# Optimization experiments

Hardware: AMD Instinct MI355X
Metric: run time of the kernel (lower is better)

Reference implementation:

```python
import jax, jax.numpy as jnp
import numpy as np

NUM_HEADS = 16
DIM = 1024
N_TOKENS = 2048
S0 = 8            # number of frames
P = N_TOKENS // S0  # tokens per frame
B = 1


def setup_inputs() -> dict:
    key = jax.random.key(0)
    ks = jax.random.split(key, 8)
    C = DIM
    x = jax.random.normal(ks[0], (B, N_TOKENS, C), dtype=jnp.float32)
    # nn.Linear-style weights (out_features, in_features), scaled ~1/sqrt(fan_in)
    Wqkv = jax.random.normal(ks[1], (3 * C, C), dtype=jnp.float32) * (C ** -0.5)
    bqkv = jnp.zeros((3 * C,), dtype=jnp.float32)
    Wproj = jax.random.normal(ks[2], (C, C), dtype=jnp.float32) * (C ** -0.5)
    bproj = jnp.zeros((C,), dtype=jnp.float32)
    frame_bias = jax.random.normal(ks[3], (S0, S0), dtype=jnp.float32) * 0.5
    # frame adjacency: random sparsity pattern, diagonal always allowed
    adj = jax.random.bernoulli(ks[4], 0.25, (S0, S0))
    adj = adj | jnp.eye(S0, dtype=bool)
    frame_ids = (jnp.arange(N_TOKENS) // P).astype(jnp.int64)
    is_hub = jax.random.bernoulli(ks[5], 0.05, (N_TOKENS,))
    return {
        'x': x, 'Wqkv': Wqkv, 'bqkv': bqkv, 'Wproj': Wproj, 'bproj': bproj,
        'frame_bias': frame_bias, 'adj': adj, 'frame_ids': frame_ids,
        'is_hub': is_hub,
    }


def _sparse_attention(x, Wqkv, bqkv, Wproj, bproj, frame_bias, adj, frame_ids, is_hub):
    Bx, N, C = x.shape
    H = NUM_HEADS
    D = C // H
    scale = D ** -0.5
    # qkv projection -> q,k,v each [B,H,N,D]
    qkv = x @ Wqkv.T + bqkv                      # [B,N,3C]
    qkv = qkv.reshape(Bx, N, 3, H, D).transpose(2, 0, 3, 1, 4)
    q, k, v = qkv[0], qkv[1], qkv[2]

    # token-level mask derived from frame-level structures (score_mod semantics)
    fi = frame_ids                               # [N]
    adj_allowed = adj[fi[:, None], fi[None, :]]  # [N,N] bool
    same_frame = fi[:, None] == fi[None, :]
    neither_hub = ~(is_hub[:, None] | is_hub[None, :])
    hub_allowed = same_frame | neither_hub       # mask_hub_tokens=True
    allowed = adj_allowed & hub_allowed
    bias = frame_bias[fi[:, None], fi[None, :]]  # soft_mask=True

    scores = jnp.einsum('bhqd,bhkd->bhqk', q, k) * scale
    scores = jnp.where(allowed, scores + bias, -jnp.inf)
    attn = jax.nn.softmax(scores, axis=-1)
    out = jnp.einsum('bhqk,bhkd->bhqd', attn, v)
    out = out.transpose(0, 2, 1, 3).reshape(Bx, N, C)
    return out @ Wproj.T + bproj


def reference(x, Wqkv, bqkv, Wproj, bproj, frame_bias, adj, frame_ids, is_hub):
    return _sparse_attention(x, Wqkv, bqkv, Wproj, bproj, frame_bias,
                             adj, frame_ids, is_hub)
```

## Files before the change

### kernel.cpp

```cpp
#include <hip/hip_runtime.h>
#include <hip/hip_bf16.h>
#include <math.h>

#define NTOK 2048
#define CDIM 1024
#define NHEAD 16
#define HDIM 64

typedef __attribute__((ext_vector_type(8))) short bf16x8;
typedef __attribute__((ext_vector_type(4))) float f32x4;
typedef __attribute__((ext_vector_type(4))) unsigned int u32x4;

__device__ inline unsigned short bf16_rn(float f) {
    unsigned int u = __float_as_uint(f);
    u += 0x7FFFu + ((u >> 16) & 1u);
    return (unsigned short)(u >> 16);
}

template <int N> __device__ inline void waitcnt_vm() {
    if constexpr (N == 0) asm volatile("s_waitcnt vmcnt(0)" ::: "memory");
    else if constexpr (N == 4) asm volatile("s_waitcnt vmcnt(4)" ::: "memory");
    else if constexpr (N == 6) asm volatile("s_waitcnt vmcnt(6)" ::: "memory");
}

__device__ inline void gload16(const void* g, void* l) {
    __builtin_amdgcn_global_load_lds((const __attribute__((address_space(1))) void*)g,
                                     (__attribute__((address_space(3))) void*)l,
                                     16, 0, 0);
}

__global__ __launch_bounds__(256) void conv3(const float* __restrict__ s0, unsigned short* __restrict__ h0, int nb0,
                                             const float* __restrict__ s1, unsigned short* __restrict__ h1, int nb1,
                                             const float* __restrict__ s2, unsigned short* __restrict__ h2) {
    int b = blockIdx.x;
    const float* s;
    unsigned short* hh;
    if (b < nb0) { s = s0; hh = h0; }
    else if (b < nb0 + nb1) { s = s1; hh = h1; b -= nb0; }
    else { s = s2; hh = h2; b -= nb0 + nb1; }
    const int i = b * 256 + threadIdx.x;
    float4 v = ((const float4*)s)[i];
    ushort4 h;
    h.x = bf16_rn(v.x); h.y = bf16_rn(v.y); h.z = bf16_rn(v.z); h.w = bf16_rn(v.w);
    ((ushort4*)hh)[i] = h;
}

template <int BM, int BN, int M, int N, int K, int MODE>
__global__ __launch_bounds__(256) void gemm_mfma(const unsigned short* __restrict__ Ah,
                                                 const unsigned short* __restrict__ Bh,
                                                 const float* __restrict__ bias,
                                                 float* __restrict__ C,
                                                 unsigned short* __restrict__ qfb,
                                                 unsigned short* __restrict__ kfb,
                                                 unsigned short* __restrict__ vfb) {
    constexpr int BK = 64;
    constexpr int FM = BM / 32;
    constexpr int FN = BN / 32;
    constexpr int ASZ = BM * BK;
    constexpr int BSZ = BN * BK;
    constexpr int BUF = ASZ + BSZ;
    __shared__ unsigned short lds[2 * BUF];

    const int tid = threadIdx.x;
    const int lane = tid & 63;
    const int w = tid >> 6;
    const int m0 = blockIdx.y * BM;
    const int n0 = blockIdx.x * BN;
    const int wave_m = (w >> 1) * (BM / 2);
    const int wave_n = (w & 1) * (BN / 2);
    const int lr = lane & 15;
    const int kg_ = lane >> 4;
    const int srow = tid >> 3;
    const int scol = (tid & 7) * 8;

    const size_t aRow = (size_t)(m0 + srow) * K + scol;
    const size_t bRow = (size_t)(n0 + srow) * K + scol;

    f32x4 acc[FM][FN];
#pragma unroll
    for (int i = 0; i < FM; ++i)
#pragma unroll
        for (int j = 0; j < FN; ++j) acc[i][j] = {0.f, 0.f, 0.f, 0.f};

    auto stage = [&](int buf, int k0) {
        unsigned short* bb = lds + buf * BUF;
#pragma unroll
        for (int j = 0; j < BM / 32; ++j)
            gload16(Ah + aRow + (size_t)j * 32 * K + k0, bb + (srow + j * 32) * BK + scol);
#pragma unroll
        for (int j = 0; j < BN / 32; ++j)
            gload16(Bh + bRow + (size_t)j * 32 * K + k0, bb + ASZ + (srow + j * 32) * BK + scol);
    };

    stage(0, 0);
    constexpr int NL = BM / 32 + BN / 32;
    constexpr int NT = K / BK;
    for (int t = 0; t < NT; ++t) {
        const int cur = t & 1;
        if (t + 1 < NT) {
            stage(cur ^ 1, (t + 1) * BK);
            waitcnt_vm<NL>();
        } else {
            waitcnt_vm<0>();
        }
        __builtin_amdgcn_s_barrier();

        const unsigned short* bb = lds + cur * BUF;
        bf16x8 ah[FM][2], bh[FN][2];
#pragma unroll
        for (int f = 0; f < FM; ++f)
#pragma unroll
            for (int ks = 0; ks < 2; ++ks)
                ah[f][ks] = *(const bf16x8*)&bb[(wave_m + f * 16 + lr) * BK + ks * 32 + kg_ * 8];
#pragma unroll
        for (int f = 0; f < FN; ++f)
#pragma unroll
            for (int ks = 0; ks < 2; ++ks)
                bh[f][ks] = *(const bf16x8*)&bb[ASZ + (wave_n + f * 16 + lr) * BK + ks * 32 + kg_ * 8];
        __builtin_amdgcn_s_setprio(1);
#pragma unroll
        for (int ks = 0; ks < 2; ++ks)
#pragma unroll
            for (int fm = 0; fm < FM; ++fm)
#pragma unroll
                for (int fn = 0; fn < FN; ++fn)
                    acc[fm][fn] = __builtin_amdgcn_mfma_f32_16x16x32_bf16(ah[fm][ks], bh[fn][ks], acc[fm][fn], 0, 0, 0);
        __builtin_amdgcn_s_setprio(0);
        asm volatile("" ::: "memory");
        __builtin_amdgcn_s_barrier();
    }

    if constexpr (MODE == 2) {
        float bv[FN];
#pragma unroll
        for (int fn = 0; fn < FN; ++fn) bv[fn] = bias[n0 + wave_n + fn * 16 + lr];
#pragma unroll
        for (int fm = 0; fm < FM; ++fm) {
            const int row0 = m0 + wave_m + fm * 16 + kg_ * 4;
#pragma unroll
            for (int fn = 0; fn < FN; ++fn) {
                const int col = n0 + wave_n + fn * 16 + lr;
#pragma unroll
                for (int r = 0; r < 4; ++r)
                    C[(size_t)(row0 + r) * N + col] = acc[fm][fn][r] + bv[fn];
            }
        }
    } else {
        const int reg = n0 >> 10;
#pragma unroll
        for (int fn = 0; fn < FN; ++fn) {
            const int col = n0 + wave_n + fn * 16 + lr;
            const int head = (col >> 6) & 15;
            const int d = col & 63;
            const float bv = bias[col];
#pragma unroll
            for (int fm = 0; fm < FM; ++fm) {
                const int row0 = m0 + wave_m + fm * 16 + kg_ * 4;
                if (reg == 2) {
                    const int tok = row0;
                    const int tile = tok >> 6;
                    const int t6 = tok & 63;
                    const int c = t6 >> 5;
                    const int t5 = t6 & 31;
                    const int hi = (t5 >> 4) & 1;
                    const int kgv = (t5 >> 2) & 3;
                    const int fd = d >> 4;
                    const int lrv = d & 15;
                    ushort4 pk;
                    pk.x = bf16_rn(acc[fm][fn][0] + bv);
                    pk.y = bf16_rn(acc[fm][fn][1] + bv);
                    pk.z = bf16_rn(acc[fm][fn][2] + bv);
                    pk.w = bf16_rn(acc[fm][fn][3] + bv);
                    const size_t idx = (((size_t)((head * 32 + tile) * 2 + c) * 4 + fd) * 64 +
                                        (kgv * 16 + lrv)) * 8 + hi * 4;
                    *(ushort4*)&vfb[idx] = pk;
                } else if (reg == 1) {
                    const int dc = d >> 5;
                    const int kgq = (d >> 3) & 3;
                    const int e = d & 7;
#pragma unroll
                    for (int r = 0; r < 4; ++r) {
                        const int tok = row0 + r;
                        const int tile = tok >> 6;
                        const int fk = (tok >> 4) & 3;
                        const int lrk = tok & 15;
                        const size_t idx = (((size_t)((head * 32 + tile) * 4 + fk) * 2 + dc) * 64 +
                                            (kgq * 16 + lrk)) * 8 + e;
                        kfb[idx] = bf16_rn(acc[fm][fn][r] + bv);
                    }
                } else {
                    const int dc = d >> 5;
                    const int kgq = (d >> 3) & 3;
                    const int e = d & 7;
#pragma unroll
                    for (int r = 0; r < 4; ++r) {
                        const int tok = row0 + r;
                        const int q16i = tok >> 4;
                        const int lrk = tok & 15;
                        const size_t idx = (((size_t)(head * 128 + q16i) * 2 + dc) * 64 +
                                            (kgq * 16 + lrk)) * 8 + e;
                        qfb[idx] = bf16_rn((acc[fm][fn][r] + bv) * 0.125f);
                    }
                }
            }
        }
    }
}

__global__ __launch_bounds__(128, 4) void attn_mfma(const unsigned short* __restrict__ qfb,
                                                    const unsigned short* __restrict__ kfb,
                                                    const unsigned short* __restrict__ vfb,
                                                    const float* __restrict__ frame_bias,
                                                    const int* __restrict__ adj,
                                                    const int* __restrict__ is_hub,
                                                    unsigned short* __restrict__ ath) {
    __shared__ float sM[64][18];
    __shared__ int sList[32];
    __shared__ float sFB[8];
    __shared__ unsigned long long sHub[32];
    __shared__ int sNT;

    const int bid = blockIdx.x;
    const int r8 = bid & 7, tt = bid >> 3;
    const int q16 = tt & 127, hb = tt >> 7;
    const int h = r8 * 2 + hb;
    const int q0 = q16 * 16;

    const int tid = threadIdx.x;
    const int lane = tid & 63;
    const int w = tid >> 6;
    const int lr = lane & 15;
    const int kg = lane >> 4;
    const int fi = q0 >> 8;

    const unsigned short* qb = qfb + ((size_t)(h * 128 + q16) * 2) * 512;
    bf16x8 qh[2];
    qh[0] = *(const bf16x8*)&qb[lane * 8];
    qh[1] = *(const bf16x8*)&qb[512 + lane * 8];
    const bool hq = is_hub[q0 + lr] != 0;

#pragma unroll
    for (int i = 0; i < 16; ++i) {
        const int t2 = w * 16 + i;
        unsigned long long mb = __ballot(is_hub[t2 * 64 + lane] != 0);
        if (lane == 0) sHub[t2] = mb;
    }
    if (tid < 8) sFB[tid] = frame_bias[fi * 8 + tid];
    if (w == 0) {
        const bool ok = (lane < 32) && (adj[fi * 8 + ((lane & 31) >> 2)] != 0);
        const unsigned long long am = __ballot(ok);
        if (lane == 0) {
            int c = 0;
#pragma unroll 1
            for (int t2 = 0; t2 < 32; ++t2)
                if ((am >> t2) & 1ull) sList[c++] = t2;
            sNT = c;
        }
    }
    __syncthreads();
    const int nt = sNT;

    const unsigned short* kb = kfb + (size_t)(h * 32) * 4096;
    const unsigned short* vb = vfb + (size_t)(h * 32) * 4096;

    float m_i = -INFINITY, l_i = 0.f;
    f32x4 oacc[4];
#pragma unroll
    for (int fd = 0; fd < 4; ++fd) oacc[fd] = {0.f, 0.f, 0.f, 0.f};

#pragma unroll 1
    for (int i = w; i < nt; i += 2) {
        const int tile = sList[i];
        const size_t tbase = (size_t)tile * 4096 + lane * 8;
        const int fj = tile >> 2;
        const bool same = (fj == fi);
        const float biasv = sFB[fj];
        const unsigned long long hubmask = sHub[tile];

        bf16x8 kfr[4][2];
#pragma unroll
        for (int fk = 0; fk < 4; ++fk)
#pragma unroll
            for (int dc = 0; dc < 2; ++dc)
                kfr[fk][dc] = *(const bf16x8*)&kb[tbase + (fk * 2 + dc) * 512];

        f32x4 sacc[4];
#pragma unroll
        for (int fk = 0; fk < 4; ++fk) sacc[fk] = {0.f, 0.f, 0.f, 0.f};
        __builtin_amdgcn_s_setprio(1);
#pragma unroll
        for (int fk = 0; fk < 4; ++fk)
#pragma unroll
            for (int dc = 0; dc < 2; ++dc)
                sacc[fk] = __builtin_amdgcn_mfma_f32_16x16x32_bf16(kfr[fk][dc], qh[dc], sacc[fk], 0, 0, 0);
        __builtin_amdgcn_s_setprio(0);

        bf16x8 vfr[2][4];
#pragma unroll
        for (int c = 0; c < 2; ++c)
#pragma unroll
            for (int fd = 0; fd < 4; ++fd)
                vfr[c][fd] = *(const bf16x8*)&vb[tbase + (c * 4 + fd) * 512];

        float sv[4][4];
        float rmax = -INFINITY;
#pragma unroll
        for (int fk = 0; fk < 4; ++fk)
#pragma unroll
            for (int r = 0; r < 4; ++r) {
                float val = sacc[fk][r] + biasv;
                if (!same) {
                    const int k = fk * 16 + kg * 4 + r;
                    if (hq || ((hubmask >> k) & 1ull)) val = -INFINITY;
                }
                sv[fk][r] = val;
                rmax = fmaxf(rmax, val);
            }
        rmax = fmaxf(rmax, __shfl_xor(rmax, 16));
        rmax = fmaxf(rmax, __shfl_xor(rmax, 32));

        if (!__all(rmax <= m_i + 8.f)) {
            const float mn = fmaxf(m_i, rmax);
            const float alpha = (m_i == -INFINITY) ? 0.f : __expf(m_i - mn);
            m_i = mn;
            l_i *= alpha;
#pragma unroll
            for (int fd = 0; fd < 4; ++fd) {
                oacc[fd][0] *= alpha; oacc[fd][1] *= alpha;
                oacc[fd][2] *= alpha; oacc[fd][3] *= alpha;
            }
        }

        float p4[4][4];
        float psum = 0.f;
#pragma unroll
        for (int fk = 0; fk < 4; ++fk)
#pragma unroll
            for (int r = 0; r < 4; ++r) {
                const float pv = (sv[fk][r] == -INFINITY) ? 0.f : __expf(sv[fk][r] - m_i);
                p4[fk][r] = pv;
                psum += pv;
            }
        psum += __shfl_xor(psum, 16);
        psum += __shfl_xor(psum, 32);
        l_i += psum;

        unsigned int pc[4][2];
#pragma unroll
        for (int fk = 0; fk < 4; ++fk)
#pragma unroll
            for (int rp = 0; rp < 2; ++rp)
                pc[fk][rp] = (unsigned int)bf16_rn(p4[fk][2 * rp]) |
                             ((unsigned int)bf16_rn(p4[fk][2 * rp + 1]) << 16);
        __builtin_amdgcn_s_setprio(1);
#pragma unroll
        for (int c = 0; c < 2; ++c) {
            u32x4 pw = {pc[2 * c][0], pc[2 * c][1], pc[2 * c + 1][0], pc[2 * c + 1][1]};
            bf16x8 pbv = __builtin_bit_cast(bf16x8, pw);
#pragma unroll
            for (int fd = 0; fd < 4; ++fd)
                oacc[fd] = __builtin_amdgcn_mfma_f32_16x16x32_bf16(vfr[c][fd], pbv, oacc[fd], 0, 0, 0);
        }
        __builtin_amdgcn_s_setprio(0);
    }

    if (w == 1) {
        float* mp = &sM[lane][0];
        mp[0] = m_i;
        mp[1] = l_i;
#pragma unroll
        for (int fd = 0; fd < 4; ++fd)
#pragma unroll
            for (int r = 0; r < 4; ++r) mp[2 + fd * 4 + r] = oacc[fd][r];
    }
    __syncthreads();
    if (w == 0) {
        const float mb = sM[lane][0];
        const float lb = sM[lane][1];
        const float m = fmaxf(m_i, mb);
        const float aa = (m_i == -INFINITY) ? 0.f : __expf(m_i - m);
        const float ab = (mb == -INFINITY) ? 0.f : __expf(mb - m);
        const float inv = 1.f / (l_i * aa + lb * ab);
#pragma unroll
        for (int fd = 0; fd < 4; ++fd) {
            ushort4 h4;
            unsigned short hs[4];
#pragma unroll
            for (int r = 0; r < 4; ++r) {
                const float o = (oacc[fd][r] * aa + sM[lane][2 + fd * 4 + r] * ab) * inv;
                hs[r] = bf16_rn(o);
            }
            h4.x = hs[0]; h4.y = hs[1]; h4.z = hs[2]; h4.w = hs[3];
            const size_t idx = (size_t)(q0 + lr) * CDIM + h * 64 + fd * 16 + kg * 4;
            *(ushort4*)&ath[idx] = h4;
        }
    }
}

extern "C" void kernel_launch(void* const* d_in, const int* in_sizes, int n_in,
                              void* d_out, int out_size, void* d_ws, size_t ws_size,
                              hipStream_t stream) {
    const float* x          = (const float*)d_in[0];
    const float* Wqkv       = (const float*)d_in[1];
    const float* bqkv       = (const float*)d_in[2];
    const float* Wproj      = (const float*)d_in[3];
    const float* bproj      = (const float*)d_in[4];
    const float* frame_bias = (const float*)d_in[5];
    const int*   adj        = (const int*)d_in[6];
    const int*   is_hub     = (const int*)d_in[8];
    float* out = (float*)d_out;

    char* ws = (char*)d_ws;
    size_t off = 0;
    auto alloc_us = [&](size_t n) { unsigned short* p = (unsigned short*)(ws + off); off += n * 2; return p; };
    unsigned short* qfb = alloc_us((size_t)NHEAD * NTOK * HDIM);
    unsigned short* kfb = alloc_us((size_t)NHEAD * NTOK * HDIM);
    unsigned short* vfb = alloc_us((size_t)NHEAD * HDIM * NTOK);
    unsigned short* xh  = alloc_us((size_t)NTOK * CDIM);
    unsigned short* wqh = alloc_us((size_t)3 * CDIM * CDIM);
    unsigned short* wph = alloc_us((size_t)CDIM * CDIM);
    unsigned short* ath = alloc_us((size_t)NTOK * CDIM);

    const int nb_x = (NTOK * CDIM / 4) / 256;
    const int nb_wq = (3 * CDIM * CDIM / 4) / 256;
    const int nb_wp = (CDIM * CDIM / 4) / 256;
    conv3<<<nb_x + nb_wq + nb_wp, 256, 0, stream>>>(x, xh, nb_x,
                                                    Wqkv, wqh, nb_wq,
                                                    Wproj, wph);

    gemm_mfma<64, 128, NTOK, 3 * CDIM, CDIM, 1>
        <<<dim3((3 * CDIM) / 128, NTOK / 64), 256, 0, stream>>>(
            xh, wqh, bqkv, nullptr, qfb, kfb, vfb);
    attn_mfma<<<2048, 128, 0, stream>>>(qfb, kfb, vfb,
                                        frame_bias, adj, is_hub, ath);
    gemm_mfma<64, 64, NTOK, CDIM, CDIM, 2>
        <<<dim3(CDIM / 64, NTOK / 64), 256, 0, stream>>>(
            ath, wph, bproj, out, nullptr, nullptr, nullptr);
}
```

Before: 70.12 us.

## Prefetch next K tile in attention loop and stage Q/K epilogue via LDS

The attention loop now double-buffers K fragments, issuing the next tile's K loads before processing the current tile so global load latency overlaps the MFMA and softmax work. Separately, the QKV GEMM epilogue for the Q and K regions first writes the fp32 results to shared memory and then emits packed 8-element bf16 vector stores, replacing scattered 2-byte stores. Both add register or LDS pressure and an extra barrier. The epilogue also assumes the LDS buffer is large enough for the staged tile.

```diff
diff --git a/kernel.cpp b/kernel.cpp
--- a/kernel.cpp
+++ b/kernel.cpp
@@ -147,17 +147,16 @@
         }
     } else {
         const int reg = n0 >> 10;
-#pragma unroll
-        for (int fn = 0; fn < FN; ++fn) {
-            const int col = n0 + wave_n + fn * 16 + lr;
-            const int head = (col >> 6) & 15;
-            const int d = col & 63;
-            const float bv = bias[col];
-#pragma unroll
-            for (int fm = 0; fm < FM; ++fm) {
-                const int row0 = m0 + wave_m + fm * 16 + kg_ * 4;
-                if (reg == 2) {
-                    const int tok = row0;
+        if (reg == 2) {
+#pragma unroll
+            for (int fn = 0; fn < FN; ++fn) {
+                const int col = n0 + wave_n + fn * 16 + lr;
+                const int head = (col >> 6) & 15;
+                const int d = col & 63;
+                const float bv = bias[col];
+#pragma unroll
+                for (int fm = 0; fm < FM; ++fm) {
+                    const int tok = m0 + wave_m + fm * 16 + kg_ * 4;
                     const int tile = tok >> 6;
                     const int t6 = tok & 63;
                     const int c = t6 >> 5;
@@ -174,34 +173,58 @@
                     const size_t idx = (((size_t)((head * 32 + tile) * 2 + c) * 4 + fd) * 64 +
                                         (kgv * 16 + lrv)) * 8 + hi * 4;
                     *(ushort4*)&vfb[idx] = pk;
-                } else if (reg == 1) {
-                    const int dc = d >> 5;
-                    const int kgq = (d >> 3) & 3;
-                    const int e = d & 7;
-#pragma unroll
-                    for (int r = 0; r < 4; ++r) {
-                        const int tok = row0 + r;
-                        const int tile = tok >> 6;
-                        const int fk = (tok >> 4) & 3;
-                        const int lrk = tok & 15;
-                        const size_t idx = (((size_t)((head * 32 + tile) * 4 + fk) * 2 + dc) * 64 +
-                                            (kgq * 16 + lrk)) * 8 + e;
-                        kfb[idx] = bf16_rn(acc[fm][fn][r] + bv);
-                    }
-                } else {
-                    const int dc = d >> 5;
-                    const int kgq = (d >> 3) & 3;
-                    const int e = d & 7;
-#pragma unroll
-                    for (int r = 0; r < 4; ++r) {
-                        const int tok = row0 + r;
-                        const int q16i = tok >> 4;
-                        const int lrk = tok & 15;
-                        const size_t idx = (((size_t)(head * 128 + q16i) * 2 + dc) * 64 +
-                                            (kgq * 16 + lrk)) * 8 + e;
-                        qfb[idx] = bf16_rn((acc[fm][fn][r] + bv) * 0.125f);
-                    }
                 }
+            }
+        } else {
+            float* sOut = (float*)lds;
+            float bv[FN];
+#pragma unroll
+            for (int fn = 0; fn < FN; ++fn) bv[fn] = bias[n0 + wave_n + fn * 16 + lr];
+#pragma unroll
+            for (int fm = 0; fm < FM; ++fm) {
+                const int row0 = wave_m + fm * 16 + kg_ * 4;
+#pragma unroll
+                for (int fn = 0; fn < FN; ++fn) {
+                    const int col = wave_n + fn * 16 + lr;
+#pragma unroll
+                    for (int r = 0; r < 4; ++r)
+                        sOut[(row0 + r) * 132 + col] = acc[fm][fn][r] + bv[fn];
+                }
+            }
+            __syncthreads();
+            const float sc = (reg == 0) ? 0.125f : 1.0f;
+            unsigned short* dp = (reg == 0) ? qfb : kfb;
+            const int tokL = tid >> 2;
+            const int tokG = m0 + tokL;
+            const int lrk = tokG & 15;
+#pragma unroll
+            for (int j = 0; j < 4; ++j) {
+                const int ch = (tid & 3) + j * 4;
+                const int dcol = ch * 8;
+                const int gcol = n0 + dcol;
+                const int head = (gcol >> 6) & 15;
+                const int d = gcol & 63;
+                const int dc = d >> 5;
+                const int kgq = (d >> 3) & 3;
+                float4 v0 = *(float4*)&sOut[tokL * 132 + dcol];
+                float4 v1 = *(float4*)&sOut[tokL * 132 + dcol + 4];
+                bf16x8 pk;
+                pk[0] = (short)bf16_rn(v0.x * sc);
+                pk[1] = (short)bf16_rn(v0.y * sc);
+                pk[2] = (short)bf16_rn(v0.z * sc);
+                pk[3] = (short)bf16_rn(v0.w * sc);
+                pk[4] = (short)bf16_rn(v1.x * sc);
+                pk[5] = (short)bf16_rn(v1.y * sc);
+                pk[6] = (short)bf16_rn(v1.z * sc);
+                pk[7] = (short)bf16_rn(v1.w * sc);
+                size_t idx;
+                if (reg == 1)
+                    idx = (((size_t)((head * 32 + (tokG >> 6)) * 4 + ((tokG >> 4) & 3)) * 2 + dc) * 64 +
+                           (kgq * 16 + lrk)) * 8;
+                else
+                    idx = (((size_t)(head * 128 + (tokG >> 4)) * 2 + dc) * 64 +
+                           (kgq * 16 + lrk)) * 8;
+                *(bf16x8*)&dp[idx] = pk;
             }
         }
     }
@@ -268,22 +291,22 @@
 #pragma unroll
     for (int fd = 0; fd < 4; ++fd) oacc[fd] = {0.f, 0.f, 0.f, 0.f};
 
-#pragma unroll 1
-    for (int i = w; i < nt; i += 2) {
-        const int tile = sList[i];
+    auto loadK = [&](bf16x8 (&kf)[4][2], int tile) {
+        const size_t tb = (size_t)tile * 4096 + lane * 8;
+#pragma unroll
+        for (int fk = 0; fk < 4; ++fk)
+#pragma unroll
+            for (int dc = 0; dc < 2; ++dc)
+                kf[fk][dc] = *(const bf16x8*)&kb[tb + (fk * 2 + dc) * 512];
+    };
+
+    auto procTile = [&](int tile, bf16x8 (&kf)[4][2]) {
         const size_t tbase = (size_t)tile * 4096 + lane * 8;
         const int fj = tile >> 2;
         const bool same = (fj == fi);
         const float biasv = sFB[fj];
         const unsigned long long hubmask = sHub[tile];
 
-        bf16x8 kfr[4][2];
-#pragma unroll
-        for (int fk = 0; fk < 4; ++fk)
-#pragma unroll
-            for (int dc = 0; dc < 2; ++dc)
-                kfr[fk][dc] = *(const bf16x8*)&kb[tbase + (fk * 2 + dc) * 512];
-
         f32x4 sacc[4];
 #pragma unroll
         for (int fk = 0; fk < 4; ++fk) sacc[fk] = {0.f, 0.f, 0.f, 0.f};
@@ -292,7 +315,7 @@
         for (int fk = 0; fk < 4; ++fk)
 #pragma unroll
             for (int dc = 0; dc < 2; ++dc)
-                sacc[fk] = __builtin_amdgcn_mfma_f32_16x16x32_bf16(kfr[fk][dc], qh[dc], sacc[fk], 0, 0, 0);
+                sacc[fk] = __builtin_amdgcn_mfma_f32_16x16x32_bf16(kf[fk][dc], qh[dc], sacc[fk], 0, 0, 0);
         __builtin_amdgcn_s_setprio(0);
 
         bf16x8 vfr[2][4];
@@ -302,7 +325,7 @@
             for (int fd = 0; fd < 4; ++fd)
                 vfr[c][fd] = *(const bf16x8*)&vb[tbase + (c * 4 + fd) * 512];
 
-        float sv[4][4];
+        float s[4][4];
         float rmax = -INFINITY;
 #pragma unroll
         for (int fk = 0; fk < 4; ++fk)
@@ -313,7 +336,7 @@
                     const int k = fk * 16 + kg * 4 + r;
                     if (hq || ((hubmask >> k) & 1ull)) val = -INFINITY;
                 }
-                sv[fk][r] = val;
+                s[fk][r] = val;
                 rmax = fmaxf(rmax, val);
             }
         rmax = fmaxf(rmax, __shfl_xor(rmax, 16));
@@ -331,14 +354,13 @@
             }
         }
 
-        float p4[4][4];
         float psum = 0.f;
 #pragma unroll
         for (int fk = 0; fk < 4; ++fk)
 #pragma unroll
             for (int r = 0; r < 4; ++r) {
-                const float pv = (sv[fk][r] == -INFINITY) ? 0.f : __expf(sv[fk][r] - m_i);
-                p4[fk][r] = pv;
+                const float pv = (s[fk][r] == -INFINITY) ? 0.f : __expf(s[fk][r] - m_i);
+                s[fk][r] = pv;
                 psum += pv;
             }
         psum += __shfl_xor(psum, 16);
@@ -350,8 +372,8 @@
         for (int fk = 0; fk < 4; ++fk)
 #pragma unroll
             for (int rp = 0; rp < 2; ++rp)
-                pc[fk][rp] = (unsigned int)bf16_rn(p4[fk][2 * rp]) |
-                             ((unsigned int)bf16_rn(p4[fk][2 * rp + 1]) << 16);
+                pc[fk][rp] = (unsigned int)bf16_rn(s[fk][2 * rp]) |
+                             ((unsigned int)bf16_rn(s[fk][2 * rp + 1]) << 16);
         __builtin_amdgcn_s_setprio(1);
 #pragma unroll
         for (int c = 0; c < 2; ++c) {
@@ -362,6 +384,21 @@
                 oacc[fd] = __builtin_amdgcn_mfma_f32_16x16x32_bf16(vfr[c][fd], pbv, oacc[fd], 0, 0, 0);
         }
         __builtin_amdgcn_s_setprio(0);
+    };
+
+    bf16x8 kA[4][2], kB[4][2];
+    loadK(kA, sList[w]);
+    int i = w;
+    while (true) {
+        const int iB = i + 2;
+        if (iB < nt) loadK(kB, sList[iB]);
+        procTile(sList[i], kA);
+        if (iB >= nt) break;
+        const int iA2 = i + 4;
+        if (iA2 < nt) loadK(kA, sList[iA2]);
+        procTile(sList[iB], kB);
+        if (iA2 >= nt) break;
+        i = iA2;
     }
 
     if (w == 1) {
```

After: 129.8 us. 85.2% more time.
